# Performance work log

Measured on AMD Instinct MI355X. Metric: run time of the kernel, lower is better.

Reference implementation:

```python
import jax, jax.numpy as jnp
import numpy as np

C = 256

def setup_inputs() -> dict:
    key = jax.random.key(0)
    ks = jax.random.split(key, 8)
    B, H, W = 4, 64, 64
    x = jax.random.normal(ks[0], (B, C, H, W), dtype=jnp.float32)
    # 1x1 conv weights ~ kaiming uniform; bias zero
    bound = np.sqrt(6.0 / C)
    Wq = jax.random.uniform(ks[1], (C, C), minval=-bound, maxval=bound, dtype=jnp.float32)
    Wk = jax.random.uniform(ks[2], (C, C), minval=-bound, maxval=bound, dtype=jnp.float32)
    Wv = jax.random.uniform(ks[3], (C, C), minval=-bound, maxval=bound, dtype=jnp.float32)
    bq = jnp.zeros((C,), jnp.float32)
    bk = jnp.zeros((C,), jnp.float32)
    bv = jnp.zeros((C,), jnp.float32)
    # gamma initialized to zero in torch; use small nonzero so output depends on attn path
    gamma = jnp.array([0.1], dtype=jnp.float32)
    return {"x": x, "Wq": Wq, "bq": bq, "Wk": Wk, "bk": bk, "Wv": Wv, "bv": bv, "gamma": gamma}


def reference(x, Wq, bq, Wk, bk, Wv, bv, gamma):
    B, Cc, H, W = x.shape
    N = H * W
    xf = x.reshape(B, Cc, N)  # [B,C,N]
    # 1x1 conv == per-pixel linear over channels: out[b,o,n] = sum_c W[o,c]*x[b,c,n] + b[o]
    q = jnp.einsum('oc,bcn->bon', Wq, xf) + bq[None, :, None]  # [B,C,N]
    k = jnp.einsum('oc,bcn->bon', Wk, xf) + bk[None, :, None]
    v = jnp.einsum('oc,bcn->bon', Wv, xf) + bv[None, :, None]
    # energy[b,i,j] = q[b,:,i] . k[b,:,j]  (no scaling, as in source)
    energy = jnp.einsum('bci,bcj->bij', q, k)  # [B,N,N]
    attention = jax.nn.softmax(energy, axis=-1)
    # out[b,c,i] = sum_j v[b,c,j] * attention[b,i,j]  (bmm(value, attn^T))
    out = jnp.einsum('bcj,bij->bci', v, attention)
    out = out.reshape(B, Cc, H, W)
    return gamma * out + x
```

## Files before the change

### kernel.cpp

```cpp
#include <hip/hip_runtime.h>
#include <hip/hip_bf16.h>
#include <cstdint>


#define C_DIM 256
#define N_DIM 4096
#define B_DIM 4

typedef _Float16 f16;
typedef f16 f16x8 __attribute__((ext_vector_type(8)));
typedef f16 f16x4 __attribute__((ext_vector_type(4)));
typedef float f32x4 __attribute__((ext_vector_type(4)));

__device__ __forceinline__ void dma16(const f16* g, f16* l) {
  __builtin_amdgcn_global_load_lds(
      (const __attribute__((address_space(1))) unsigned int*)g,
      (__attribute__((address_space(3))) unsigned int*)l, 16, 0, 0);
}

__global__ __launch_bounds__(256) void k_cast_w(const float* __restrict__ Wq,
                                                const float* __restrict__ Wk,
                                                const float* __restrict__ Wv,
                                                f16* __restrict__ Wh) {
  int i = blockIdx.x * 256 + threadIdx.x;
  int sel = i >> 16, j = i & 65535;
  const float* s = (sel == 0) ? Wq : (sel == 1) ? Wk : Wv;
  Wh[i] = (f16)s[j];
}

__global__ __launch_bounds__(512) void k_qkv(const float* __restrict__ x,
                                             const f16* __restrict__ Wh,
                                             const float* __restrict__ bq,
                                             const float* __restrict__ bk,
                                             const float* __restrict__ bv,
                                             f16* __restrict__ Qh,
                                             f16* __restrict__ Kh,
                                             f16* __restrict__ Vh) {
  __shared__ __align__(16) f16 xt[64 * 256];
  const int b = blockIdx.y, n0 = blockIdx.x * 64;
  const int tid = threadIdx.x;
  const int w = tid >> 6, lane = tid & 63;
  const int quad = lane >> 4, li = lane & 15;
  const int gt = w & 3, role = w >> 2;

  {
    const float* xb = x + (size_t)b * C_DIM * N_DIM + n0;
#pragma unroll
    for (int cg = 0; cg < 4; cg++) {
      f16x8 v;
#pragma unroll
      for (int j = 0; j < 8; j++) {
        int c = w * 32 + cg * 8 + j;
        v[j] = (f16)xb[(size_t)c * N_DIM + lane];
      }
      int chunk = w * 4 + cg;
      int slot = chunk ^ (lane & 7);
      *(f16x8*)(&xt[lane * 256 + slot * 8]) = v;
    }
  }
  __syncthreads();

  int xsl[8];
#pragma unroll
  for (int kf = 0; kf < 8; kf++) xsl[kf] = ((kf * 4 + quad) ^ (li & 7)) << 3;
  f16x8 xf[8];
  {
    const f16* xrow = xt + (gt * 16 + li) * 256;
#pragma unroll
    for (int kf = 0; kf < 8; kf++) xf[kf] = *(const f16x8*)(xrow + xsl[kf]);
  }

  {
    const f16* W = Wh + (size_t)role * 65536;
    const float* bias = role ? bk : bq;
    f16* out = role ? Kh : Qh;
    const size_t grow = (size_t)(b * N_DIM + n0 + gt * 16 + li) * C_DIM;
    for (int ot = 0; ot < 16; ot++) {
      f32x4 acc = {0.f, 0.f, 0.f, 0.f};
      const f16* wrow = W + (size_t)(ot * 16 + li) * C_DIM + quad * 8;
#pragma unroll
      for (int kf = 0; kf < 8; kf++) {
        f16x8 wf = *(const f16x8*)(wrow + kf * 32);
        acc = __builtin_amdgcn_mfma_f32_16x16x32_f16(wf, xf[kf], acc, 0, 0, 0);
      }
      const int o0 = ot * 16 + quad * 4;
      f16x4 st = {(f16)(acc[0] + bias[o0]), (f16)(acc[1] + bias[o0 + 1]),
                  (f16)(acc[2] + bias[o0 + 2]), (f16)(acc[3] + bias[o0 + 3])};
      *(f16x4*)(out + grow + o0) = st;
    }
  }

  {
    const f16* W = Wh + (size_t)2 * 65536;
#pragma unroll
    for (int ot8 = 0; ot8 < 8; ot8++) {
      const int ot = role * 8 + ot8;
      f32x4 acc = {0.f, 0.f, 0.f, 0.f};
      const f16* wrow = W + (size_t)(ot * 16 + li) * C_DIM + quad * 8;
#pragma unroll
      for (int kf = 0; kf < 8; kf++) {
        f16x8 wf = *(const f16x8*)(wrow + kf * 32);
        acc = __builtin_amdgcn_mfma_f32_16x16x32_f16(xf[kf], wf, acc, 0, 0, 0);
      }
      const float bb = bv[ot * 16 + li];
      f16x4 st = {(f16)(acc[0] + bb), (f16)(acc[1] + bb),
                  (f16)(acc[2] + bb), (f16)(acc[3] + bb)};
      *(f16x4*)(Vh + (size_t)(b * C_DIM + ot * 16 + li) * N_DIM +
                n0 + gt * 16 + quad * 4) = st;
    }
  }
}

#define JT 64
#define NT (N_DIM / JT)
#define K0_OFF 0
#define K1_OFF 16384
#define V0_OFF 32768
#define V1_OFF 49152
#define P_OFF  65536
#define PSTR 40
#define SMEM_F16 70656
#define MRG_WSTR 4160
#define MRG_CSTR 260
#define ML_OFF   16640

__global__ __launch_bounds__(512, 1) void k_attn(const f16* __restrict__ Qh,
                                                 const f16* __restrict__ Kh,
                                                 const f16* __restrict__ Vh,
                                                 const float* __restrict__ x,
                                                 const float* __restrict__ gamma_p,
                                                 float* __restrict__ out) {
  __shared__ __align__(16) f16 smem[SMEM_F16];
  const int b = blockIdx.y;
  const int tid = threadIdx.x;
  const int w = tid >> 6, lane = tid & 63;
  const int wq = w & 3, wj = w >> 2;
  const int quad = lane >> 4, li = lane & 15;
  const int lw = li & 7;
  const int ibase = blockIdx.x * 64 + wq * 16;

  int ksl[8];
#pragma unroll
  for (int kf = 0; kf < 8; kf++) ksl[kf] = ((kf * 4 + quad) ^ lw) << 3;
  const int vsl = ((wj * 4 + quad) ^ lw) << 3;

  f16x8 qf[8];
  {
    const f16* qrow = Qh + (size_t)(b * N_DIM + ibase + li) * C_DIM + quad * 8;
#pragma unroll
    for (int kf = 0; kf < 8; kf++) qf[kf] = *(const f16x8*)(qrow + kf * 32);
  }
  const f16* Kb = Kh + (size_t)b * N_DIM * C_DIM;
  const f16* Vb = Vh + (size_t)b * C_DIM * N_DIM;
  f16* Pw = smem + P_OFF + w * 16 * PSTR;

  const float LOG2E = 1.4426950408889634f;
  float m = -3.0e38f, l = 0.0f;
  f32x4 acc[16];
#pragma unroll
  for (int ct = 0; ct < 16; ct++) acc[ct] = (f32x4){0.f, 0.f, 0.f, 0.f};

  {
#pragma unroll
    for (int it = 0; it < 4; it++) {
      int p = w * 4 + it;
      int krsw = (2 * it + (lane >> 5)) & 7;
      dma16(Kb + (size_t)(2 * p + (lane >> 5)) * C_DIM + (((lane & 31) ^ krsw) * 8),
            smem + K0_OFF + p * 512);
      dma16(Vb + (size_t)(p * 8 + (lane >> 3)) * N_DIM + (((lane & 7) ^ (lane >> 3)) * 8),
            smem + V0_OFF + p * 512);
    }
  }
  __syncthreads();

  for (int t = 0; t < NT; t++) {
    const f16* Kc = smem + ((t & 1) ? K1_OFF : K0_OFF);
    const f16* Vc = smem + ((t & 1) ? V1_OFF : V0_OFF);

    if (t + 1 < NT) {
      f16* Kn = smem + ((t & 1) ? K0_OFF : K1_OFF);
      f16* Vn = smem + ((t & 1) ? V0_OFF : V1_OFF);
      const int jt = (t + 1) * JT;
      const f16* kg = Kb + (size_t)jt * C_DIM;
      const f16* vg = Vb + jt;
#pragma unroll
      for (int it = 0; it < 4; it++) {
        int p = w * 4 + it;
        int krsw = (2 * it + (lane >> 5)) & 7;
        dma16(kg + (size_t)(2 * p + (lane >> 5)) * C_DIM + (((lane & 31) ^ krsw) * 8),
              Kn + p * 512);
        dma16(vg + (size_t)(p * 8 + (lane >> 3)) * N_DIM + (((lane & 7) ^ (lane >> 3)) * 8),
              Vn + p * 512);
      }
    }

    f32x4 s[2];
#pragma unroll
    for (int sub = 0; sub < 2; sub++) {
      f32x4 ss = {0.f, 0.f, 0.f, 0.f};
      const f16* krow = Kc + (wj * 32 + sub * 16 + li) * 256;
#pragma unroll
      for (int kf = 0; kf < 8; kf++) {
        f16x8 kfr = *(const f16x8*)(krow + ksl[kf]);
        ss = __builtin_amdgcn_mfma_f32_16x16x32_f16(kfr, qf[kf], ss, 0, 0, 0);
      }
      s[sub] = ss;
    }

    float tm = fmaxf(fmaxf(fmaxf(s[0][0], s[0][1]), fmaxf(s[0][2], s[0][3])),
                     fmaxf(fmaxf(s[1][0], s[1][1]), fmaxf(s[1][2], s[1][3])));
    tm = fmaxf(tm, __shfl_xor(tm, 16));
    tm = fmaxf(tm, __shfl_xor(tm, 32));
    float nm = fmaxf(m, tm);
    float alpha = exp2f((m - nm) * LOG2E);
    m = nm;
    if (__any(alpha < 1.0f)) {
      l *= alpha;
#pragma unroll
      for (int ct = 0; ct < 16; ct++) {
        acc[ct][0] *= alpha; acc[ct][1] *= alpha;
        acc[ct][2] *= alpha; acc[ct][3] *= alpha;
      }
    }
#pragma unroll
    for (int sub = 0; sub < 2; sub++) {
      float p0 = exp2f((s[sub][0] - m) * LOG2E);
      float p1 = exp2f((s[sub][1] - m) * LOG2E);
      float p2 = exp2f((s[sub][2] - m) * LOG2E);
      float p3 = exp2f((s[sub][3] - m) * LOG2E);
      l += (p0 + p1) + (p2 + p3);
      *(f16x4*)(Pw + li * PSTR + sub * 16 + quad * 4) =
          (f16x4){(f16)p0, (f16)p1, (f16)p2, (f16)p3};
    }

    f16x8 pf = *(const f16x8*)(Pw + li * PSTR + quad * 8);
#pragma unroll
    for (int ct = 0; ct < 16; ct++) {
      const f16* vrow = Vc + (ct * 16 + li) * 64;
      f16x8 v = *(const f16x8*)(vrow + vsl);
      acc[ct] = __builtin_amdgcn_mfma_f32_16x16x32_f16(v, pf, acc[ct], 0, 0, 0);
    }

    __syncthreads();
  }

  l += __shfl_xor(l, 16);
  l += __shfl_xor(l, 32);

  float* mrg = (float*)smem;
  if (wj == 1) {
    const int u = wq;
    float* base = mrg + u * MRG_WSTR + li * MRG_CSTR;
#pragma unroll
    for (int ct = 0; ct < 16; ct++)
      *(f32x4*)(base + ct * 16 + quad * 4) = acc[ct];
    if (lane < 16) {
      mrg[ML_OFF + u * 32 + li] = m;
      mrg[ML_OFF + u * 32 + 16 + li] = l;
    }
  }
  __syncthreads();
  if (wj == 0) {
    const int u = wq;
    const float m_b = mrg[ML_OFF + u * 32 + li];
    const float l_b = mrg[ML_OFF + u * 32 + 16 + li];
    const float M = fmaxf(m, m_b);
    const float aa = exp2f((m - M) * LOG2E);
    const float ab = exp2f((m_b - M) * LOG2E);
    const float lm = aa * l + ab * l_b;
    const float scale = gamma_p[0] / lm;
    const float* base = mrg + u * MRG_WSTR + li * MRG_CSTR;

    const float* xb = x + (size_t)b * C_DIM * N_DIM;
    float* ob = out + (size_t)b * C_DIM * N_DIM;
    const int icol = ibase + li;
#pragma unroll
    for (int ct = 0; ct < 16; ct++) {
      f32x4 accb = *(const f32x4*)(base + ct * 16 + quad * 4);
#pragma unroll
      for (int r = 0; r < 4; r++) {
        size_t off = (size_t)(ct * 16 + quad * 4 + r) * N_DIM + icol;
        ob[off] = (acc[ct][r] * aa + accb[r] * ab) * scale + xb[off];
      }
    }
  }
}

extern "C" void kernel_launch(void* const* d_in, const int* in_sizes, int n_in,
                              void* d_out, int out_size, void* d_ws, size_t ws_size,
                              hipStream_t stream) {
  const float* x     = (const float*)d_in[0];
  const float* Wq    = (const float*)d_in[1];
  const float* bq    = (const float*)d_in[2];
  const float* Wk    = (const float*)d_in[3];
  const float* bk    = (const float*)d_in[4];
  const float* Wv    = (const float*)d_in[5];
  const float* bv    = (const float*)d_in[6];
  const float* gamma = (const float*)d_in[7];
  float* out = (float*)d_out;

  char* ws = (char*)d_ws;
  f16* Qh = (f16*)(ws);
  f16* Kh = (f16*)(ws + (size_t)8  * 1024 * 1024);
  f16* Vh = (f16*)(ws + (size_t)16 * 1024 * 1024);
  f16* Wh = (f16*)(ws + (size_t)24 * 1024 * 1024);

  k_cast_w<<<dim3(768), 256, 0, stream>>>(Wq, Wk, Wv, Wh);
  k_qkv<<<dim3(64, 4), 512, 0, stream>>>(x, Wh, bq, bk, bv, Qh, Kh, Vh);
  k_attn<<<dim3(64, 4), 512, 0, stream>>>(Qh, Kh, Vh, x, gamma, out);
}
```

Measured before the change: 250.2 us.

## Split attention waves 2x4 over query/key, keep P in registers, 4-way merge

Reorganizes the attention kernel so each wave handles 32 query rows (two 16-row tiles) against 16 keys of the 64-key tile, instead of 16 queries against 32 keys. Each K fragment is now reused across two Q tiles. The P matrix no longer goes through LDS: the 16x16x16 MFMA consumes the exp results directly from registers, which removes the P shared-memory round trip. The final merge combines four partial softmax states per query group in two LDS passes. Launch bounds now request 2 blocks per CU, which doubles the accumulator registers per wave and may cause spills or limit occupancy.

```diff
diff --git a/kernel.cpp b/kernel.cpp
--- a/kernel.cpp
+++ b/kernel.cpp
@@ -117,14 +117,12 @@
 #define K1_OFF 16384
 #define V0_OFF 32768
 #define V1_OFF 49152
-#define P_OFF  65536
-#define PSTR 40
-#define SMEM_F16 70656
-#define MRG_WSTR 4160
-#define MRG_CSTR 260
-#define ML_OFF   16640
-
-__global__ __launch_bounds__(512, 1) void k_attn(const f16* __restrict__ Qh,
+#define SMEM_F16 65536
+#define MRG_SLOT 4224
+#define MRG_ISTR 132
+#define ML_OFF   25344
+
+__global__ __launch_bounds__(512, 2) void k_attn(const f16* __restrict__ Qh,
                                                  const f16* __restrict__ Kh,
                                                  const f16* __restrict__ Vh,
                                                  const float* __restrict__ x,
@@ -134,31 +132,37 @@
   const int b = blockIdx.y;
   const int tid = threadIdx.x;
   const int w = tid >> 6, lane = tid & 63;
-  const int wq = w & 3, wj = w >> 2;
+  const int wq = w & 1, wj = w >> 1;
   const int quad = lane >> 4, li = lane & 15;
   const int lw = li & 7;
-  const int ibase = blockIdx.x * 64 + wq * 16;
+  const int ibase = blockIdx.x * 64 + wq * 32;
 
   int ksl[8];
 #pragma unroll
   for (int kf = 0; kf < 8; kf++) ksl[kf] = ((kf * 4 + quad) ^ lw) << 3;
-  const int vsl = ((wj * 4 + quad) ^ lw) << 3;
-
-  f16x8 qf[8];
-  {
-    const f16* qrow = Qh + (size_t)(b * N_DIM + ibase + li) * C_DIM + quad * 8;
-#pragma unroll
-    for (int kf = 0; kf < 8; kf++) qf[kf] = *(const f16x8*)(qrow + kf * 32);
+  const int vofs = (((wj * 2 + (quad >> 1)) ^ lw) << 3) + (quad & 1) * 4;
+
+  f16x8 qf0[8], qf1[8];
+  {
+    const f16* qrow0 = Qh + (size_t)(b * N_DIM + ibase + li) * C_DIM + quad * 8;
+    const f16* qrow1 = qrow0 + (size_t)16 * C_DIM;
+#pragma unroll
+    for (int kf = 0; kf < 8; kf++) {
+      qf0[kf] = *(const f16x8*)(qrow0 + kf * 32);
+      qf1[kf] = *(const f16x8*)(qrow1 + kf * 32);
+    }
   }
   const f16* Kb = Kh + (size_t)b * N_DIM * C_DIM;
   const f16* Vb = Vh + (size_t)b * C_DIM * N_DIM;
-  f16* Pw = smem + P_OFF + w * 16 * PSTR;
 
   const float LOG2E = 1.4426950408889634f;
-  float m = -3.0e38f, l = 0.0f;
-  f32x4 acc[16];
-#pragma unroll
-  for (int ct = 0; ct < 16; ct++) acc[ct] = (f32x4){0.f, 0.f, 0.f, 0.f};
+  float m0 = -3.0e38f, l0 = 0.0f, m1 = -3.0e38f, l1 = 0.0f;
+  f32x4 acc[16][2];
+#pragma unroll
+  for (int ct = 0; ct < 16; ct++) {
+    acc[ct][0] = (f32x4){0.f, 0.f, 0.f, 0.f};
+    acc[ct][1] = (f32x4){0.f, 0.f, 0.f, 0.f};
+  }
 
   {
 #pragma unroll
@@ -194,93 +198,148 @@
       }
     }
 
-    f32x4 s[2];
-#pragma unroll
-    for (int sub = 0; sub < 2; sub++) {
-      f32x4 ss = {0.f, 0.f, 0.f, 0.f};
-      const f16* krow = Kc + (wj * 32 + sub * 16 + li) * 256;
+    f32x4 s0 = {0.f, 0.f, 0.f, 0.f}, s1 = {0.f, 0.f, 0.f, 0.f};
+    {
+      const f16* krow = Kc + (wj * 16 + li) * 256;
 #pragma unroll
       for (int kf = 0; kf < 8; kf++) {
         f16x8 kfr = *(const f16x8*)(krow + ksl[kf]);
-        ss = __builtin_amdgcn_mfma_f32_16x16x32_f16(kfr, qf[kf], ss, 0, 0, 0);
-      }
-      s[sub] = ss;
-    }
-
-    float tm = fmaxf(fmaxf(fmaxf(s[0][0], s[0][1]), fmaxf(s[0][2], s[0][3])),
-                     fmaxf(fmaxf(s[1][0], s[1][1]), fmaxf(s[1][2], s[1][3])));
-    tm = fmaxf(tm, __shfl_xor(tm, 16));
-    tm = fmaxf(tm, __shfl_xor(tm, 32));
-    float nm = fmaxf(m, tm);
-    float alpha = exp2f((m - nm) * LOG2E);
-    m = nm;
-    if (__any(alpha < 1.0f)) {
-      l *= alpha;
+        s0 = __builtin_amdgcn_mfma_f32_16x16x32_f16(kfr, qf0[kf], s0, 0, 0, 0);
+        s1 = __builtin_amdgcn_mfma_f32_16x16x32_f16(kfr, qf1[kf], s1, 0, 0, 0);
+      }
+    }
+
+    float tm0 = fmaxf(fmaxf(s0[0], s0[1]), fmaxf(s0[2], s0[3]));
+    float tm1 = fmaxf(fmaxf(s1[0], s1[1]), fmaxf(s1[2], s1[3]));
+    tm0 = fmaxf(tm0, __shfl_xor(tm0, 16));
+    tm0 = fmaxf(tm0, __shfl_xor(tm0, 32));
+    tm1 = fmaxf(tm1, __shfl_xor(tm1, 16));
+    tm1 = fmaxf(tm1, __shfl_xor(tm1, 32));
+    float nm0 = fmaxf(m0, tm0), nm1 = fmaxf(m1, tm1);
+    float a0 = exp2f((m0 - nm0) * LOG2E);
+    float a1 = exp2f((m1 - nm1) * LOG2E);
+    m0 = nm0; m1 = nm1;
+    if (__any(a0 < 1.0f || a1 < 1.0f)) {
+      l0 *= a0; l1 *= a1;
 #pragma unroll
       for (int ct = 0; ct < 16; ct++) {
-        acc[ct][0] *= alpha; acc[ct][1] *= alpha;
-        acc[ct][2] *= alpha; acc[ct][3] *= alpha;
-      }
-    }
-#pragma unroll
-    for (int sub = 0; sub < 2; sub++) {
-      float p0 = exp2f((s[sub][0] - m) * LOG2E);
-      float p1 = exp2f((s[sub][1] - m) * LOG2E);
-      float p2 = exp2f((s[sub][2] - m) * LOG2E);
-      float p3 = exp2f((s[sub][3] - m) * LOG2E);
-      l += (p0 + p1) + (p2 + p3);
-      *(f16x4*)(Pw + li * PSTR + sub * 16 + quad * 4) =
-          (f16x4){(f16)p0, (f16)p1, (f16)p2, (f16)p3};
-    }
-
-    f16x8 pf = *(const f16x8*)(Pw + li * PSTR + quad * 8);
+        acc[ct][0][0] *= a0; acc[ct][0][1] *= a0;
+        acc[ct][0][2] *= a0; acc[ct][0][3] *= a0;
+        acc[ct][1][0] *= a1; acc[ct][1][1] *= a1;
+        acc[ct][1][2] *= a1; acc[ct][1][3] *= a1;
+      }
+    }
+    float p00 = exp2f((s0[0] - m0) * LOG2E), p01 = exp2f((s0[1] - m0) * LOG2E);
+    float p02 = exp2f((s0[2] - m0) * LOG2E), p03 = exp2f((s0[3] - m0) * LOG2E);
+    float p10 = exp2f((s1[0] - m1) * LOG2E), p11 = exp2f((s1[1] - m1) * LOG2E);
+    float p12 = exp2f((s1[2] - m1) * LOG2E), p13 = exp2f((s1[3] - m1) * LOG2E);
+    l0 += (p00 + p01) + (p02 + p03);
+    l1 += (p10 + p11) + (p12 + p13);
+    f16x4 pf0 = {(f16)p00, (f16)p01, (f16)p02, (f16)p03};
+    f16x4 pf1 = {(f16)p10, (f16)p11, (f16)p12, (f16)p13};
+
 #pragma unroll
     for (int ct = 0; ct < 16; ct++) {
       const f16* vrow = Vc + (ct * 16 + li) * 64;
-      f16x8 v = *(const f16x8*)(vrow + vsl);
-      acc[ct] = __builtin_amdgcn_mfma_f32_16x16x32_f16(v, pf, acc[ct], 0, 0, 0);
+      f16x4 va = *(const f16x4*)(vrow + vofs);
+      acc[ct][0] = __builtin_amdgcn_mfma_f32_16x16x16f16(va, pf0, acc[ct][0], 0, 0, 0);
+      acc[ct][1] = __builtin_amdgcn_mfma_f32_16x16x16f16(va, pf1, acc[ct][1], 0, 0, 0);
     }
 
     __syncthreads();
   }
 
-  l += __shfl_xor(l, 16);
-  l += __shfl_xor(l, 32);
+  l0 += __shfl_xor(l0, 16); l0 += __shfl_xor(l0, 32);
+  l1 += __shfl_xor(l1, 16); l1 += __shfl_xor(l1, 32);
 
   float* mrg = (float*)smem;
-  if (wj == 1) {
-    const int u = wq;
-    float* base = mrg + u * MRG_WSTR + li * MRG_CSTR;
-#pragma unroll
-    for (int ct = 0; ct < 16; ct++)
-      *(f32x4*)(base + ct * 16 + quad * 4) = acc[ct];
-    if (lane < 16) {
-      mrg[ML_OFF + u * 32 + li] = m;
-      mrg[ML_OFF + u * 32 + 16 + li] = l;
-    }
-  }
-  __syncthreads();
+  const int uid = wq * 3 + (wj - 1);
+  if (wj != 0) {
+    if (quad == 0)
+      *(f32x4*)(mrg + ML_OFF + (uid * 16 + li) * 4) = (f32x4){m0, m1, l0, l1};
+    float* base = mrg + uid * MRG_SLOT;
+#pragma unroll
+    for (int c8 = 0; c8 < 8; c8++) {
+      *(f32x4*)(base + (li) * MRG_ISTR + c8 * 16 + quad * 4) = acc[c8][0];
+      *(f32x4*)(base + (16 + li) * MRG_ISTR + c8 * 16 + quad * 4) = acc[c8][1];
+    }
+  }
+  __syncthreads();
+
+  float es0 = 0.f, es1 = 0.f, e0[3], e1[3], scale0 = 0.f, scale1 = 0.f;
   if (wj == 0) {
-    const int u = wq;
-    const float m_b = mrg[ML_OFF + u * 32 + li];
-    const float l_b = mrg[ML_OFF + u * 32 + 16 + li];
-    const float M = fmaxf(m, m_b);
-    const float aa = exp2f((m - M) * LOG2E);
-    const float ab = exp2f((m_b - M) * LOG2E);
-    const float lm = aa * l + ab * l_b;
-    const float scale = gamma_p[0] / lm;
-    const float* base = mrg + u * MRG_WSTR + li * MRG_CSTR;
-
-    const float* xb = x + (size_t)b * C_DIM * N_DIM;
-    float* ob = out + (size_t)b * C_DIM * N_DIM;
-    const int icol = ibase + li;
-#pragma unroll
-    for (int ct = 0; ct < 16; ct++) {
-      f32x4 accb = *(const f32x4*)(base + ct * 16 + quad * 4);
+    f32x4 mlp[3];
+#pragma unroll
+    for (int k = 0; k < 3; k++)
+      mlp[k] = *(const f32x4*)(mrg + ML_OFF + ((wq * 3 + k) * 16 + li) * 4);
+    float M0 = fmaxf(fmaxf(m0, mlp[0][0]), fmaxf(mlp[1][0], mlp[2][0]));
+    float M1 = fmaxf(fmaxf(m1, mlp[0][1]), fmaxf(mlp[1][1], mlp[2][1]));
+    es0 = exp2f((m0 - M0) * LOG2E);
+    es1 = exp2f((m1 - M1) * LOG2E);
+    float L0 = es0 * l0, L1 = es1 * l1;
+#pragma unroll
+    for (int k = 0; k < 3; k++) {
+      e0[k] = exp2f((mlp[k][0] - M0) * LOG2E);
+      e1[k] = exp2f((mlp[k][1] - M1) * LOG2E);
+      L0 += e0[k] * mlp[k][2];
+      L1 += e1[k] * mlp[k][3];
+    }
+    const float g = gamma_p[0];
+    scale0 = g / L0; scale1 = g / L1;
+  }
+
+  const float* xb = x + (size_t)b * C_DIM * N_DIM;
+  float* ob = out + (size_t)b * C_DIM * N_DIM;
+  const int icol0 = ibase + li, icol1 = ibase + 16 + li;
+
+  if (wj == 0) {
+#pragma unroll
+    for (int c8 = 0; c8 < 8; c8++) {
+      f32x4 v0 = acc[c8][0], v1 = acc[c8][1];
+      v0 *= es0; v1 *= es1;
+#pragma unroll
+      for (int k = 0; k < 3; k++) {
+        const float* base = mrg + (wq * 3 + k) * MRG_SLOT;
+        f32x4 q0 = *(const f32x4*)(base + li * MRG_ISTR + c8 * 16 + quad * 4);
+        f32x4 q1 = *(const f32x4*)(base + (16 + li) * MRG_ISTR + c8 * 16 + quad * 4);
+        v0 += e0[k] * q0; v1 += e1[k] * q1;
+      }
 #pragma unroll
       for (int r = 0; r < 4; r++) {
-        size_t off = (size_t)(ct * 16 + quad * 4 + r) * N_DIM + icol;
-        ob[off] = (acc[ct][r] * aa + accb[r] * ab) * scale + xb[off];
+        size_t off0 = (size_t)(c8 * 16 + quad * 4 + r) * N_DIM;
+        ob[off0 + icol0] = v0[r] * scale0 + xb[off0 + icol0];
+        ob[off0 + icol1] = v1[r] * scale1 + xb[off0 + icol1];
+      }
+    }
+  }
+  __syncthreads();
+
+  if (wj != 0) {
+    float* base = mrg + uid * MRG_SLOT;
+#pragma unroll
+    for (int c8 = 0; c8 < 8; c8++) {
+      *(f32x4*)(base + li * MRG_ISTR + c8 * 16 + quad * 4) = acc[8 + c8][0];
+      *(f32x4*)(base + (16 + li) * MRG_ISTR + c8 * 16 + quad * 4) = acc[8 + c8][1];
+    }
+  }
+  __syncthreads();
+  if (wj == 0) {
+#pragma unroll
+    for (int c8 = 0; c8 < 8; c8++) {
+      f32x4 v0 = acc[8 + c8][0], v1 = acc[8 + c8][1];
+      v0 *= es0; v1 *= es1;
+#pragma unroll
+      for (int k = 0; k < 3; k++) {
+        const float* base = mrg + (wq * 3 + k) * MRG_SLOT;
+        f32x4 q0 = *(const f32x4*)(base + li * MRG_ISTR + c8 * 16 + quad * 4);
+        f32x4 q1 = *(const f32x4*)(base + (16 + li) * MRG_ISTR + c8 * 16 + quad * 4);
+        v0 += e0[k] * q0; v1 += e1[k] * q1;
+      }
+#pragma unroll
+      for (int r = 0; r < 4; r++) {
+        size_t off0 = (size_t)(128 + c8 * 16 + quad * 4 + r) * N_DIM;
+        ob[off0 + icol0] = v0[r] * scale0 + xb[off0 + icol0];
+        ob[off0 + icol1] = v1[r] * scale1 + xb[off0 + icol1];
       }
     }
   }
```

New measurement: 273.8 us. 1.09x slower.
